# Kernel optimization log

Hardware: AMD Instinct MI355X
Metric: run time of the kernel (lower is better)

Reference implementation:

```python
import jax, jax.numpy as jnp
import numpy as np
from jax import lax

B, L, D, VOCAB = 4, 256, 256, 29


def conv1d(x, w, b, pad, stride=1):
    # x: (B, C, Len), w: (O, I, K)
    y = lax.conv_general_dilated(x, w, (stride,), [pad], dimension_numbers=('NCH', 'OIH', 'NCH'))
    return y + b[None, :, None]


def setup_inputs() -> dict:
    key = jax.random.key(0)
    ks = jax.random.split(key, 14)
    n = lambda k, shape: jax.random.normal(k, shape, jnp.float32) * 0.05
    return {
        'prot_data1': jax.random.randint(ks[0], (B, L), 0, VOCAB),
        'prot_data2': jax.random.randint(ks[1], (B, L), 0, VOCAB),
        'emb': n(ks[2], (VOCAB, D)),
        'w0': n(ks[3], (D, D, 4)), 'b0': jnp.zeros((D,), jnp.float32),
        'w1': n(ks[4], (D, D, 8)), 'b1': jnp.zeros((D,), jnp.float32),
        'w2': n(ks[5], (D, D, 12)), 'b2': jnp.zeros((D,), jnp.float32),
        'ja1_w': n(ks[6], (D, D)), 'ja1_b': jnp.zeros((D,), jnp.float32),
        'ja2_w': n(ks[7], (D, D)), 'ja2_b': jnp.zeros((D,), jnp.float32),
        'rc_w': n(ks[8], (64, 1, 4)), 'rc_b': jnp.zeros((64,), jnp.float32),
        'fc1_w': n(ks[9], (64 * 32, 600)), 'fc1_b': jnp.zeros((600,), jnp.float32),
        'fc2_w': n(ks[10], (600, 300)), 'fc2_b': jnp.zeros((300,), jnp.float32),
        'fc3_w': n(ks[11], (300, 1)), 'fc3_b': jnp.zeros((1,), jnp.float32),
    }


def reference(prot_data1, prot_data2, emb, w0, b0, w1, b1, w2, b2,
              ja1_w, ja1_b, ja2_w, ja2_b, rc_w, rc_b,
              fc1_w, fc1_b, fc2_w, fc2_b, fc3_w, fc3_b):
    lrelu = lambda x: jnp.where(x >= 0, x, 0.1 * x)

    def encode(tok):
        x = emb[tok]  # (B, L, D); dim 1 is treated as conv channels, as in original
        x = jax.nn.relu(conv1d(x, w0, b0, (1, 2)))
        x = jax.nn.relu(conv1d(x, w1, b1, (3, 4)))
        x = jax.nn.relu(conv1d(x, w2, b2, (5, 6)))
        return x  # (B, L, D), length preserved

    e1 = encode(prot_data1)
    e2 = encode(prot_data2)

    q = jax.nn.relu(e1) @ ja1_w + ja1_b  # (B, L, D)
    k = jax.nn.relu(e2) @ ja2_w + ja2_b  # (B, L, D)
    inter = jax.nn.sigmoid(jnp.einsum('bij,bkj->bik', q, k))  # (B, L, L)
    inter = inter / jnp.sum(inter, axis=(1, 2), keepdims=True)

    # bilinear cross-attention pooling: tanh outer product weighted by inter
    pp = jnp.tanh(e1[:, :, None, :] * e2[:, None, :, :])  # (B, L, L, D)
    pooled = jnp.einsum('bikj,bik->bj', pp, inter)  # (B, D)

    h = lrelu(conv1d(pooled[:, None, :], rc_w, rc_b, (1, 1), stride=2))  # (B, 64, 128)
    h = h.reshape(h.shape[0], 64, 32, 4).max(axis=-1)  # MaxPool1d(4,4) -> (B, 64, 32)
    h = h.reshape(h.shape[0], 64 * 32)
    h = lrelu(h @ fc1_w + fc1_b)
    h = lrelu(h @ fc2_w + fc2_b)
    affn = h @ fc3_w + fc3_b  # (B, 1)
    return (inter, affn)
```

## Files before the change

kernel.cpp:

```cpp
#include <hip/hip_runtime.h>
#include <hip/hip_bf16.h>

typedef unsigned short u16;
typedef unsigned int u32;
typedef short s8v __attribute__((ext_vector_type(8)));
typedef float f32x16 __attribute__((ext_vector_type(16)));

constexpr int B = 4, L = 256, D = 256;
constexpr size_t SZ = (size_t)B * L * D;

constexpr int XROWS = 272;
constexpr size_t XT_PLANE = (size_t)8 * XROWS * 256;

constexpr size_t OFF_E    = 0;
constexpr size_t OFF_S    = 2 * SZ;
constexpr size_t OFF_EBF  = 3 * SZ;
constexpr size_t OFF_XA   = 4 * SZ;
constexpr size_t OFF_XB   = OFF_XA + 278528;
constexpr size_t OFF_WB   = OFF_XB + 278528;
constexpr size_t OFF_WJ   = OFF_WB + 1572864;
constexpr size_t OFF_QK   = OFF_WJ + 131072;
constexpr size_t OFF_BS   = OFF_QK + 262144;
constexpr size_t OFF_PP   = OFF_BS + 256;
constexpr size_t OFF_POOL = OFF_PP + 524288;
constexpr size_t OFF_H    = OFF_POOL + 1024;
constexpr size_t OFF_F1P  = OFF_H + 8192;
constexpr size_t OFF_F2P  = OFF_F1P + 76800;

constexpr size_t WB_L1 = 0;
constexpr size_t WB_L2 = (size_t)4 * 2 * 65536;
constexpr size_t WB_L3 = WB_L2 + (size_t)8 * 2 * 65536;

__device__ __forceinline__ float sig_fast(float x) {
  return __fdividef(1.0f, 1.0f + __expf(-x));
}
__device__ __forceinline__ float lrelu(float x) { return x >= 0.0f ? x : 0.1f * x; }

__device__ __forceinline__ void split_bf16(float v, u16& h, u16& l) {
  __bf16 hb = (__bf16)v;
  float hf = (float)hb;
  __bf16 lb = (__bf16)(v - hf);
  h = __builtin_bit_cast(u16, hb);
  l = __builtin_bit_cast(u16, lb);
}
__device__ __forceinline__ u16 to_bf16(float v) {
  return __builtin_bit_cast(u16, (__bf16)v);
}

__device__ __forceinline__ s8v lds16_8al(const u16* p) {
  union { uint2 u[2]; s8v v; } r;
  r.u[0] = *(const uint2*)p;
  r.u[1] = *(const uint2*)(p + 4);
  return r.v;
}

__global__ __launch_bounds__(256) void k_prepall(const int* __restrict__ t1,
                                                 const int* __restrict__ t2,
                                                 const float* __restrict__ emb,
                                                 const float* __restrict__ w0,
                                                 const float* __restrict__ w1,
                                                 const float* __restrict__ w2,
                                                 const float* __restrict__ jw1,
                                                 const float* __restrict__ jw2,
                                                 u16* __restrict__ xa,
                                                 u16* __restrict__ xb,
                                                 u16* __restrict__ wb,
                                                 u16* __restrict__ wj) {
  __shared__ float st[32][129];
  int blk = blockIdx.x;
  int t = threadIdx.x;
  if (blk < 64) {
    int gid = blk * 256 + t;
    int plane = gid >> 13, rem = gid & 8191;
    int pb = rem >> 10, rem2 = rem & 1023;
    int row16 = rem2 >> 6, cc = rem2 & 63;
    int row = row16 < 8 ? row16 : 256 + row16;
    u16* dst = plane ? xb : xa;
    *(ushort4*)(dst + (size_t)pb * (XROWS * 256) + (size_t)row * 256 + cc * 4) =
        make_ushort4(0, 0, 0, 0);
  } else if (blk < 896) {
    int b2 = blk - 64;
    if (b2 < 768) {
      const float* w; u16* dst; int K, lblk;
      if (b2 < 128) { w = w0; dst = wb + WB_L1; K = 4; lblk = b2; }
      else if (b2 < 384) { w = w1; dst = wb + WB_L2; K = 8; lblk = b2 - 128; }
      else { w = w2; dst = wb + WB_L3; K = 12; lblk = b2 - 384; }
      int q = lblk >> 5, ig = lblk & 31, oc = t;
      union { u16 us[8]; uint4 v; } H, Lo;
#pragma unroll
      for (int e = 0; e < 8; ++e) {
        float v = w[((size_t)oc * 256 + ig * 8 + e) * K + q];
        split_bf16(v, H.us[e], Lo.us[e]);
      }
      size_t d = (size_t)(q * 2) * 65536 + (size_t)ig * 2048 + (size_t)oc * 8;
      *(uint4*)(dst + d) = H.v;
      *(uint4*)(dst + d + 65536) = Lo.v;
    } else {
      int lblk = b2 - 768;
      int kg = lblk & 31, p = lblk >> 5;
      const float* W = p ? jw2 : jw1;
      int n = t;
      union { u16 us[8]; uint4 v; } H, Lo;
#pragma unroll
      for (int e = 0; e < 8; ++e) {
        float v = W[(size_t)(kg * 8 + e) * 256 + n];
        split_bf16(v, H.us[e], Lo.us[e]);
      }
      size_t d = (size_t)(p * 2) * 65536 + ((size_t)kg * 256 + n) * 8;
      *(uint4*)(wj + d) = H.v;
      *(uint4*)(wj + d + 65536) = Lo.v;
    }
  } else {
    int lb = blk - 896;
    int dt = lb & 1, lt = (lb >> 1) & 7, pb = lb >> 4;
    int l0 = lt * 32, d0 = dt * 128;
    const int* tok = (pb >> 2) ? t2 : t1;
    int c = t & 127, rq = t >> 7;
#pragma unroll 4
    for (int rr = 0; rr < 16; ++rr) {
      int r = rr * 2 + rq;
      int tv = tok[(pb & 3) * 256 + l0 + r];
      st[r][c] = emb[(size_t)tv * 256 + d0 + c];
    }
    __syncthreads();
    int dloc = t >> 1, lq = t & 1;
    size_t rbase = (size_t)pb * (XROWS * 256) + (size_t)(8 + d0 + dloc) * 256 + l0 + lq * 16;
#pragma unroll
    for (int lh = 0; lh < 4; ++lh) {
      u16 hb[4];
#pragma unroll
      for (int cc = 0; cc < 4; ++cc)
        hb[cc] = to_bf16(st[lq * 16 + lh * 4 + cc][dloc]);
      *(ushort4*)(xa + rbase + lh * 4) = make_ushort4(hb[0], hb[1], hb[2], hb[3]);
    }
  }
}

template <int K, int P, int OUTMODE>
__global__ __launch_bounds__(256, 4) void k_cmf(const u16* __restrict__ xh,
                                                const u16* __restrict__ wb,
                                                const float* __restrict__ bias,
                                                u16* __restrict__ yh,
                                                float* __restrict__ eout,
                                                u16* __restrict__ ebf) {
  __shared__ u16 xs[12480];

  int blk = blockIdx.x;
  int jt = blk & 7, oct = (blk >> 3) & 7, pb = blk >> 6;
  int oc0 = oct * 32, j0 = jt * 32;
  int tid = threadIdx.x;
  int lane = tid & 63, wv = tid >> 6;
  int l31 = lane & 31, lhi = lane >> 5;

  {
    const u32* sh = (const u32*)(xh + (size_t)pb * (XROWS * 256) + (size_t)j0 * 256);
    u32* xd = (u32*)xs;
    for (int idx = tid; idx < 3072; idx += 256) {
      int r = idx >> 6, c2 = (idx & 63) * 2;
      *(uint2*)(xd + r * 130 + c2) = *(const uint2*)(sh + (size_t)r * 128 + c2);
    }
  }
  __syncthreads();

  f32x16 acc = {};
  size_t abase = (size_t)(oc0 + l31) * 8 + (size_t)(wv * 8 + lhi) * 2048;
  int ib0 = wv * 64 + 8 * lhi;

  for (int q = 0; q < K; ++q) {
    int jr = l31 + q + (8 - P);
    const u16* bh0 = xs + jr * 260 + ib0;
    size_t aq = (size_t)q * 131072 + abase;
#pragma unroll
    for (int ic = 0; ic < 4; ++ic) {
      s8v ah = *(const s8v*)(wb + aq + ic * 4096);
      s8v al = *(const s8v*)(wb + aq + 65536 + ic * 4096);
      s8v bh = lds16_8al(bh0 + ic * 16);
      acc = __builtin_amdgcn_mfma_f32_32x32x16_bf16(ah, bh, acc, 0, 0, 0);
      acc = __builtin_amdgcn_mfma_f32_32x32x16_bf16(al, bh, acc, 0, 0, 0);
    }
  }

  __syncthreads();
  float* cd = (float*)xs;
  int j = l31;
  if (wv > 0) {
#pragma unroll
    for (int r = 0; r < 16; ++r) {
      int ocr = (r & 3) + 8 * (r >> 2) + 4 * lhi;
      cd[(wv - 1) * 1024 + ocr * 32 + j] = acc[r];
    }
  }
  __syncthreads();
  if (wv == 0) {
#pragma unroll
    for (int r = 0; r < 16; ++r) {
      int ocr = (r & 3) + 8 * (r >> 2) + 4 * lhi;
      int idx = ocr * 32 + j;
      float s = acc[r] + cd[idx] + cd[1024 + idx] + cd[2048 + idx] + bias[oc0 + ocr];
      cd[3072 + ocr * 33 + j] = fmaxf(s, 0.0f);
    }
  }
  __syncthreads();

  if constexpr (OUTMODE == 0) {
    int jj = tid & 31, oq = tid >> 5;
    u16 hb[4];
#pragma unroll
    for (int c2 = 0; c2 < 4; ++c2)
      hb[c2] = to_bf16(cd[3072 + (oq * 4 + c2) * 33 + jj]);
    size_t ro = (size_t)pb * (XROWS * 256) + (size_t)(8 + j0 + jj) * 256 + oc0 + oq * 4;
    *(ushort4*)(yh + ro) = make_ushort4(hb[0], hb[1], hb[2], hb[3]);
  } else {
    int jj = tid & 31, oq = tid >> 5;
#pragma unroll
    for (int c2 = 0; c2 < 4; ++c2)
      eout[(size_t)pb * 65536 + (size_t)(oc0 + oq * 4 + c2) * 256 + j0 + jj] =
          cd[3072 + (oq * 4 + c2) * 33 + jj];
    int ocl = tid >> 3, dg = tid & 7;
    u16 hb[4];
#pragma unroll
    for (int c2 = 0; c2 < 4; ++c2)
      hb[c2] = to_bf16(cd[3072 + ocl * 33 + dg * 4 + c2]);
    size_t ro2 = ((size_t)pb * 256 + oc0 + ocl) * 256 + j0 + dg * 4;
    *(ushort4*)(ebf + ro2) = make_ushort4(hb[0], hb[1], hb[2], hb[3]);
  }
}

__global__ __launch_bounds__(256) void k_jam(const u16* __restrict__ ebf,
                                             const u16* __restrict__ wj,
                                             const float* __restrict__ b1,
                                             const float* __restrict__ b2,
                                             u16* __restrict__ qk) {
  __shared__ float cd[3072 + 1056];
  int blk = blockIdx.x;
  int nt = blk & 7, it = (blk >> 3) & 7, pb = blk >> 6;
  int p = pb >> 2;
  int i0 = it * 32, n0 = nt * 32;
  int tid = threadIdx.x, wv = tid >> 6, lane = tid & 63;
  int l31 = lane & 31, lhi = lane >> 5;

  const u16* eh = ebf + ((size_t)pb * 256 + i0 + l31) * 256 + lhi * 8;
  const u16* wjh = wj + (size_t)(p * 2) * 65536;

  f32x16 acc = {};
#pragma unroll
  for (int c = 0; c < 4; ++c) {
    int kc = wv * 4 + c;
    int kg = kc * 2 + lhi;
    s8v ah = *(const s8v*)(eh + kc * 16);
    s8v bh = *(const s8v*)(wjh + ((size_t)kg * 256 + n0 + l31) * 8);
    s8v bl = *(const s8v*)(wjh + 65536 + ((size_t)kg * 256 + n0 + l31) * 8);
    acc = __builtin_amdgcn_mfma_f32_32x32x16_bf16(ah, bh, acc, 0, 0, 0);
    acc = __builtin_amdgcn_mfma_f32_32x32x16_bf16(ah, bl, acc, 0, 0, 0);
  }

  if (wv > 0) {
#pragma unroll
    for (int r = 0; r < 16; ++r) {
      int row = (r & 3) + 8 * (r >> 2) + 4 * lhi;
      cd[(wv - 1) * 1024 + row * 32 + l31] = acc[r];
    }
  }
  __syncthreads();
  if (wv == 0) {
    float bv = (p ? b2 : b1)[n0 + l31];
#pragma unroll
    for (int r = 0; r < 16; ++r) {
      int row = (r & 3) + 8 * (r >> 2) + 4 * lhi;
      int idx = row * 32 + l31;
      cd[3072 + row * 33 + l31] = acc[r] + cd[idx] + cd[1024 + idx] + cd[2048 + idx] + bv;
    }
  }
  __syncthreads();

  int row = tid & 31, c8 = tid >> 5;
  u16 hb[4];
#pragma unroll
  for (int cc = 0; cc < 4; ++cc)
    hb[cc] = to_bf16(cd[3072 + row * 33 + c8 * 4 + cc]);
  size_t ro = ((size_t)pb * 256 + i0 + row) * 256 + n0 + c8 * 4;
  *(ushort4*)(qk + ro) = make_ushort4(hb[0], hb[1], hb[2], hb[3]);
}

__global__ __launch_bounds__(256) void k_scoresm(const u16* __restrict__ qk,
                                                 float* __restrict__ S,
                                                 float* __restrict__ bsums) {
  __shared__ float cd[3072 + 1056];
  int blk = blockIdx.x;
  int jt = blk & 7, it = (blk >> 3) & 7, b = blk >> 6;
  int i0 = it * 32, j0 = jt * 32;
  int tid = threadIdx.x, wv = tid >> 6, lane = tid & 63;
  int l31 = lane & 31, lhi = lane >> 5;

  const u16* qh = qk + ((size_t)b * 256 + i0 + l31) * 256 + lhi * 8;
  const u16* kh = qk + ((size_t)(4 + b) * 256 + j0 + l31) * 256 + lhi * 8;

  f32x16 acc = {};
#pragma unroll
  for (int c = 0; c < 4; ++c) {
    int kc = wv * 4 + c;
    s8v a = *(const s8v*)(qh + kc * 16);
    s8v bb = *(const s8v*)(kh + kc * 16);
    acc = __builtin_amdgcn_mfma_f32_32x32x16_bf16(a, bb, acc, 0, 0, 0);
  }

  if (wv > 0) {
#pragma unroll
    for (int r = 0; r < 16; ++r) {
      int row = (r & 3) + 8 * (r >> 2) + 4 * lhi;
      cd[(wv - 1) * 1024 + row * 32 + l31] = acc[r];
    }
  }
  __syncthreads();
  if (wv == 0) {
    float psum = 0.0f;
#pragma unroll
    for (int r = 0; r < 16; ++r) {
      int row = (r & 3) + 8 * (r >> 2) + 4 * lhi;
      int idx = row * 32 + l31;
      float s = sig_fast(acc[r] + cd[idx] + cd[1024 + idx] + cd[2048 + idx]);
      psum += s;
      cd[3072 + row * 33 + l31] = s;
    }
    for (int off = 32; off; off >>= 1) psum += __shfl_down(psum, off, 64);
    if (lane == 0) bsums[blk] = psum;
  }
  __syncthreads();

  int row = tid & 31, c8 = tid >> 5;
  float4 v;
  v.x = cd[3072 + row * 33 + c8 * 4 + 0];
  v.y = cd[3072 + row * 33 + c8 * 4 + 1];
  v.z = cd[3072 + row * 33 + c8 * 4 + 2];
  v.w = cd[3072 + row * 33 + c8 * 4 + 3];
  *(float4*)(S + ((size_t)b * 256 + i0 + row) * 256 + j0 + c8 * 4) = v;
}

__global__ __launch_bounds__(256) void k_norm(const float* __restrict__ S,
                                              const float* __restrict__ bsums,
                                              float* __restrict__ inter_out) {
  int blk = blockIdx.x;
  int b = blk >> 6;
  __shared__ float inv_s;
  int t = threadIdx.x;
  if (t < 64) {
    float v = bsums[b * 64 + t];
    for (int off = 32; off; off >>= 1) v += __shfl_down(v, off, 64);
    if (t == 0) inv_s = 1.0f / v;
  }
  __syncthreads();
  float inv = inv_s;
  size_t base = (size_t)blk * 1024 + (size_t)t * 4;
  float4 v = *(const float4*)(S + base);
  v.x *= inv; v.y *= inv; v.z *= inv; v.w *= inv;
  *(float4*)(inter_out + base) = v;
}

__global__ __launch_bounds__(256) void k_pool(const float* __restrict__ e1,
                                              const float* __restrict__ e2,
                                              const float* __restrict__ S,
                                              const float* __restrict__ bsums,
                                              float* __restrict__ pp) {
  int blk = blockIdx.x;
  int kch = blk & 15, ich = (blk >> 4) & 31, b = blk >> 9;
  int d = threadIdx.x, i0 = ich * 8, k0 = kch * 16;
  __shared__ float s2[16][8];
  __shared__ float red[128];
  __shared__ float ssp_s, tot_s;
  int t = threadIdx.x;
  if (t < 64) {
    float v = bsums[b * 64 + t];
    for (int off = 32; off; off >>= 1) v += __shfl_down(v, off, 64);
    if (t == 0) tot_s = v;
  }
  if (t < 128) {
    int ii = t >> 4, kk = t & 15;
    float v = S[((size_t)(b * 256 + i0 + ii)) * 256 + k0 + kk];
    s2[kk][ii] = 2.0f * v;
    red[t] = v;
  }
  __syncthreads();
  for (int st = 64; st; st >>= 1) {
    if (t < st) red[t] += red[t + st];
    __syncthreads();
  }
  if (t == 0) ssp_s = red[0];
  __syncthreads();

  constexpr float C2L = 2.8853900817779268f;
  float ev2[8];
#pragma unroll
  for (int ii = 0; ii < 8; ++ii)
    ev2[ii] = e1[((size_t)(b * L + i0 + ii)) * D + d] * C2L;

  float a0 = 0.f, a1 = 0.f, a2 = 0.f, a3 = 0.f;
  for (int kk = 0; kk < 16; ++kk) {
    float e2v = e2[((size_t)(b * L + k0 + kk)) * D + d];
    float s2r[8];
    *(float4*)&s2r[0] = *(const float4*)&s2[kk][0];
    *(float4*)&s2r[4] = *(const float4*)&s2[kk][4];
#pragma unroll
    for (int ii = 0; ii < 8; ++ii) {
      float r = __builtin_amdgcn_rcpf(__builtin_exp2f(ev2[ii] * e2v) + 1.0f);
      if ((ii & 3) == 0) a0 = fmaf(r, s2r[ii], a0);
      else if ((ii & 3) == 1) a1 = fmaf(r, s2r[ii], a1);
      else if ((ii & 3) == 2) a2 = fmaf(r, s2r[ii], a2);
      else a3 = fmaf(r, s2r[ii], a3);
    }
  }
  float res = (ssp_s - (a0 + a1 + a2 + a3)) * (1.0f / tot_s);
  pp[(((size_t)b * 32 + ich) * 16 + kch) * 256 + d] = res;
}

__global__ __launch_bounds__(256) void k_poolcomb(const float* __restrict__ pp,
                                                  float* __restrict__ pooled) {
  int blk = blockIdx.x;
  int dt = blk & 7, b = blk >> 3;
  int t = threadIdx.x, dl = t & 31, mg = t >> 5;
  int d = dt * 32 + dl;
  float s = 0.f;
#pragma unroll
  for (int m = 0; m < 64; ++m)
    s += pp[((size_t)b * 512 + mg * 64 + m) * 256 + d];
  __shared__ float red[8][32];
  red[mg][dl] = s;
  __syncthreads();
  if (mg == 0) {
    float tot = red[0][dl] + red[1][dl] + red[2][dl] + red[3][dl] +
                red[4][dl] + red[5][dl] + red[6][dl] + red[7][dl];
    pooled[b * 256 + d] = tot;
  }
}

__global__ __launch_bounds__(256) void k_head1(const float* __restrict__ pooled,
                                               const float* __restrict__ rcw,
                                               const float* __restrict__ rcb,
                                               float* __restrict__ h) {
  int ms = blockIdx.x;
  __shared__ float spb[4][258];
  int t = threadIdx.x;
#pragma unroll
  for (int s = 0; s < 4; ++s) {
    int idx = s * 256 + t;
    spb[idx >> 8][(idx & 255) + 1] = pooled[idx];
  }
  if (t < 4) { spb[t][0] = 0.0f; spb[t][257] = 0.0f; }
  __syncthreads();
  int b = t >> 6, c = t & 63;
  float w0 = rcw[c * 4 + 0], w1 = rcw[c * 4 + 1], w2 = rcw[c * 4 + 2], w3 = rcw[c * 4 + 3];
  float bias = rcb[c];
#pragma unroll
  for (int mm = 0; mm < 4; ++mm) {
    int m = ms * 4 + mm;
    float mx = -1e30f;
#pragma unroll
    for (int r = 0; r < 4; ++r) {
      int p2 = 2 * (4 * m + r);
      float y = bias;
      y = fmaf(w0, spb[b][p2], y);
      y = fmaf(w1, spb[b][p2 + 1], y);
      y = fmaf(w2, spb[b][p2 + 2], y);
      y = fmaf(w3, spb[b][p2 + 3], y);
      mx = fmaxf(mx, lrelu(y));
    }
    h[(size_t)(b * 64 + c) * 32 + m] = mx;
  }
}

__global__ __launch_bounds__(256) void k_fc1(const float* __restrict__ h,
                                             const float* __restrict__ w,
                                             float* __restrict__ f1p) {
  int blk = blockIdx.x;
  int ich = blk & 31, ot = blk >> 5;
  int t = threadIdx.x, ol = t & 63, b = t >> 6;
  int o = ot * 64 + ol;
  int oc_ = o < 600 ? o : 599;
  const float* hb = h + (size_t)b * 2048 + ich * 64;
  const float* wb = w + (size_t)(ich * 64) * 600 + oc_;
  float a0 = 0.f, a1 = 0.f, a2 = 0.f, a3 = 0.f;
#pragma unroll 4
  for (int i = 0; i < 64; i += 4) {
    a0 = fmaf(hb[i], wb[(size_t)i * 600], a0);
    a1 = fmaf(hb[i + 1], wb[(size_t)(i + 1) * 600], a1);
    a2 = fmaf(hb[i + 2], wb[(size_t)(i + 2) * 600], a2);
    a3 = fmaf(hb[i + 3], wb[(size_t)(i + 3) * 600], a3);
  }
  if (o < 600) f1p[((size_t)ich * 4 + b) * 600 + o] = a0 + a1 + a2 + a3;
}

__global__ __launch_bounds__(256) void k_fc2(const float* __restrict__ f1p,
                                             const float* __restrict__ fc1b,
                                             const float* __restrict__ w,
                                             float* __restrict__ f2p) {
  int blk = blockIdx.x;
  int is = blk & 7, ot = blk >> 3;
  __shared__ float h1s[4][76];
  int t = threadIdx.x;
  for (int e = t; e < 300; e += 256) {
    int bb = e / 75, ii = e % 75;
    int i = is * 75 + ii;
    float s = fc1b[i];
#pragma unroll
    for (int ich = 0; ich < 32; ++ich) s += f1p[((size_t)ich * 4 + bb) * 600 + i];
    h1s[bb][ii] = lrelu(s);
  }
  __syncthreads();
  int ol = t & 63, b = t >> 6;
  int o = ot * 64 + ol, oc_ = o < 300 ? o : 299;
  const float* wb = w + (size_t)(is * 75) * 300 + oc_;
  float a0 = 0.f, a1 = 0.f, a2 = 0.f;
#pragma unroll 5
  for (int ii = 0; ii < 75; ii += 3) {
    a0 = fmaf(h1s[b][ii], wb[(size_t)ii * 300], a0);
    a1 = fmaf(h1s[b][ii + 1], wb[(size_t)(ii + 1) * 300], a1);
    a2 = fmaf(h1s[b][ii + 2], wb[(size_t)(ii + 2) * 300], a2);
  }
  if (o < 300) f2p[((size_t)is * 4 + b) * 300 + o] = a0 + a1 + a2;
}

__global__ __launch_bounds__(1024) void k_fc3f(const float* __restrict__ f2p,
                                               const float* __restrict__ fc2b,
                                               const float* __restrict__ w3,
                                               const float* __restrict__ fc3b,
                                               float* __restrict__ out) {
  __shared__ float h2s[4][304];
  int t = threadIdx.x;
  for (int e = t; e < 1200; e += 1024) {
    int o = e % 300, b = e / 300;
    float s = fc2b[o];
#pragma unroll
    for (int is = 0; is < 8; ++is) s += f2p[((size_t)is * 4 + b) * 300 + o];
    h2s[b][o] = lrelu(s);
  }
  __syncthreads();
  int wv = t >> 6, l = t & 63;
  if (wv < 4) {
    float s = 0.f;
#pragma unroll
    for (int m = 0; m < 5; ++m) {
      int i = m * 64 + l;
      if (i < 300) s = fmaf(h2s[wv][i], w3[i], s);
    }
    for (int off = 32; off; off >>= 1) s += __shfl_down(s, off, 64);
    if (l == 0) out[262144 + wv] = s + fc3b[0];
  }
}

extern "C" void kernel_launch(void* const* d_in, const int* in_sizes, int n_in,
                              void* d_out, int out_size, void* d_ws, size_t ws_size,
                              hipStream_t stream) {
  float* ws = (float*)d_ws;
  const int* p1 = (const int*)d_in[0];
  const int* p2 = (const int*)d_in[1];
  const float* emb  = (const float*)d_in[2];
  const float* w0   = (const float*)d_in[3];
  const float* b0   = (const float*)d_in[4];
  const float* w1   = (const float*)d_in[5];
  const float* b1   = (const float*)d_in[6];
  const float* w2   = (const float*)d_in[7];
  const float* b2   = (const float*)d_in[8];
  const float* ja1w = (const float*)d_in[9];
  const float* ja1b = (const float*)d_in[10];
  const float* ja2w = (const float*)d_in[11];
  const float* ja2b = (const float*)d_in[12];
  const float* rcw  = (const float*)d_in[13];
  const float* rcb  = (const float*)d_in[14];
  const float* fc1w = (const float*)d_in[15];
  const float* fc1b = (const float*)d_in[16];
  const float* fc2w = (const float*)d_in[17];
  const float* fc2b = (const float*)d_in[18];
  const float* fc3w = (const float*)d_in[19];
  const float* fc3b = (const float*)d_in[20];
  float* out = (float*)d_out;

  u16* xa  = (u16*)(ws + OFF_XA);
  u16* xb  = (u16*)(ws + OFF_XB);
  u16* wbu = (u16*)(ws + OFF_WB);
  u16* wju = (u16*)(ws + OFF_WJ);
  u16* ebf = (u16*)(ws + OFF_EBF);
  u16* qk  = (u16*)(ws + OFF_QK);

  k_prepall<<<1024, 256, 0, stream>>>(p1, p2, emb, w0, w1, w2, ja1w, ja2w, xa, xb, wbu, wju);

  k_cmf<4, 1, 0><<<512, 256, 0, stream>>>(xa, wbu + WB_L1, b0, xb, nullptr, nullptr);
  k_cmf<8, 3, 0><<<512, 256, 0, stream>>>(xb, wbu + WB_L2, b1, xa, nullptr, nullptr);
  k_cmf<12, 5, 1><<<512, 256, 0, stream>>>(xa, wbu + WB_L3, b2, nullptr, ws + OFF_E, ebf);

  k_jam<<<512, 256, 0, stream>>>(ebf, wju, ja1b, ja2b, qk);
  k_scoresm<<<256, 256, 0, stream>>>(qk, ws + OFF_S, ws + OFF_BS);
  k_norm<<<256, 256, 0, stream>>>(ws + OFF_S, ws + OFF_BS, out);

  k_pool<<<2048, 256, 0, stream>>>(ws + OFF_E, ws + OFF_E + SZ, ws + OFF_S, ws + OFF_BS,
                                   ws + OFF_PP);
  k_poolcomb<<<32, 256, 0, stream>>>(ws + OFF_PP, ws + OFF_POOL);

  k_head1<<<8, 256, 0, stream>>>(ws + OFF_POOL, rcw, rcb, ws + OFF_H);
  k_fc1<<<320, 256, 0, stream>>>(ws + OFF_H, fc1w, ws + OFF_F1P);
  k_fc2<<<40, 256, 0, stream>>>(ws + OFF_F1P, fc1b, fc2w, ws + OFF_F2P);
  k_fc3f<<<1, 1024, 0, stream>>>(ws + OFF_F2P, fc2b, fc3w, fc3b, out);
}
```

Before: 101.1 us.

## Fuse normalization into pooling kernel and restructure conv LDS staging per wave

Removes the separate k_norm launch by having k_pool write the normalized interaction matrix for the tile it already reads. In k_cmf, each wave now loads only its own input-channel slice into a private LDS region, so the post-load block barrier is replaced by a local waitcnt. The epilogue writes results straight from registers instead of bouncing them through a second LDS transpose. Launch bounds drop from 4 to 2 blocks per CU, which gives more registers but may reduce occupancy, and the direct per-element ebf/eout stores are less coalesced.

```diff
diff --git a/kernel.cpp b/kernel.cpp
--- a/kernel.cpp
+++ b/kernel.cpp
@@ -137,13 +137,14 @@
 }
 
 template <int K, int P, int OUTMODE>
-__global__ __launch_bounds__(256, 4) void k_cmf(const u16* __restrict__ xh,
+__global__ __launch_bounds__(256, 2) void k_cmf(const u16* __restrict__ xh,
                                                 const u16* __restrict__ wb,
                                                 const float* __restrict__ bias,
                                                 u16* __restrict__ yh,
                                                 float* __restrict__ eout,
                                                 u16* __restrict__ ebf) {
-  __shared__ u16 xs[12480];
+  __shared__ u16 xsl[4 * 3264];
+  __shared__ float cd[3072];
 
   int blk = blockIdx.x;
   int jt = blk & 7, oct = (blk >> 3) & 7, pb = blk >> 6;
@@ -153,22 +154,25 @@
   int l31 = lane & 31, lhi = lane >> 5;
 
   {
-    const u32* sh = (const u32*)(xh + (size_t)pb * (XROWS * 256) + (size_t)j0 * 256);
-    u32* xd = (u32*)xs;
-    for (int idx = tid; idx < 3072; idx += 256) {
-      int r = idx >> 6, c2 = (idx & 63) * 2;
-      *(uint2*)(xd + r * 130 + c2) = *(const uint2*)(sh + (size_t)r * 128 + c2);
-    }
-  }
-  __syncthreads();
+    const u16* src = xh + (size_t)pb * (XROWS * 256) + (size_t)j0 * 256 + wv * 64;
+    u16* dst = xsl + wv * 3264;
+#pragma unroll
+    for (int it2 = 0; it2 < 12; ++it2) {
+      int e = it2 * 64 + lane;
+      int r = e >> 4, c4 = (e & 15) * 4;
+      *(uint2*)(dst + r * 68 + c4) = *(const uint2*)(src + (size_t)r * 256 + c4);
+    }
+  }
+  asm volatile("s_waitcnt lgkmcnt(0)" ::: "memory");
+  __builtin_amdgcn_sched_barrier(0);
 
   f32x16 acc = {};
   size_t abase = (size_t)(oc0 + l31) * 8 + (size_t)(wv * 8 + lhi) * 2048;
-  int ib0 = wv * 64 + 8 * lhi;
+  const u16* wslice = xsl + wv * 3264 + 8 * lhi;
 
   for (int q = 0; q < K; ++q) {
     int jr = l31 + q + (8 - P);
-    const u16* bh0 = xs + jr * 260 + ib0;
+    const u16* bh0 = wslice + jr * 68;
     size_t aq = (size_t)q * 131072 + abase;
 #pragma unroll
     for (int ic = 0; ic < 4; ++ic) {
@@ -180,49 +184,39 @@
     }
   }
 
-  __syncthreads();
-  float* cd = (float*)xs;
-  int j = l31;
   if (wv > 0) {
 #pragma unroll
     for (int r = 0; r < 16; ++r) {
       int ocr = (r & 3) + 8 * (r >> 2) + 4 * lhi;
-      cd[(wv - 1) * 1024 + ocr * 32 + j] = acc[r];
+      cd[(wv - 1) * 1024 + ocr * 32 + l31] = acc[r];
     }
   }
   __syncthreads();
   if (wv == 0) {
+    float v[16];
 #pragma unroll
     for (int r = 0; r < 16; ++r) {
       int ocr = (r & 3) + 8 * (r >> 2) + 4 * lhi;
-      int idx = ocr * 32 + j;
-      float s = acc[r] + cd[idx] + cd[1024 + idx] + cd[2048 + idx] + bias[oc0 + ocr];
-      cd[3072 + ocr * 33 + j] = fmaxf(s, 0.0f);
-    }
-  }
-  __syncthreads();
-
-  if constexpr (OUTMODE == 0) {
-    int jj = tid & 31, oq = tid >> 5;
-    u16 hb[4];
-#pragma unroll
-    for (int c2 = 0; c2 < 4; ++c2)
-      hb[c2] = to_bf16(cd[3072 + (oq * 4 + c2) * 33 + jj]);
-    size_t ro = (size_t)pb * (XROWS * 256) + (size_t)(8 + j0 + jj) * 256 + oc0 + oq * 4;
-    *(ushort4*)(yh + ro) = make_ushort4(hb[0], hb[1], hb[2], hb[3]);
-  } else {
-    int jj = tid & 31, oq = tid >> 5;
-#pragma unroll
-    for (int c2 = 0; c2 < 4; ++c2)
-      eout[(size_t)pb * 65536 + (size_t)(oc0 + oq * 4 + c2) * 256 + j0 + jj] =
-          cd[3072 + (oq * 4 + c2) * 33 + jj];
-    int ocl = tid >> 3, dg = tid & 7;
-    u16 hb[4];
-#pragma unroll
-    for (int c2 = 0; c2 < 4; ++c2)
-      hb[c2] = to_bf16(cd[3072 + ocl * 33 + dg * 4 + c2]);
-    size_t ro2 = ((size_t)pb * 256 + oc0 + ocl) * 256 + j0 + dg * 4;
-    *(ushort4*)(ebf + ro2) = make_ushort4(hb[0], hb[1], hb[2], hb[3]);
+      int idx = ocr * 32 + l31;
+      v[r] = fmaxf(acc[r] + cd[idx] + cd[1024 + idx] + cd[2048 + idx] + bias[oc0 + ocr], 0.0f);
+    }
+    if constexpr (OUTMODE == 0) {
+      size_t ro = (size_t)pb * (XROWS * 256) + (size_t)(8 + j0 + l31) * 256 + oc0 + 4 * lhi;
+#pragma unroll
+      for (int rq = 0; rq < 4; ++rq) {
+        *(ushort4*)(yh + ro + 8 * rq) =
+            make_ushort4(to_bf16(v[rq * 4 + 0]), to_bf16(v[rq * 4 + 1]),
+                         to_bf16(v[rq * 4 + 2]), to_bf16(v[rq * 4 + 3]));
+      }
+    } else {
+#pragma unroll
+      for (int r = 0; r < 16; ++r) {
+        int ocr = (r & 3) + 8 * (r >> 2) + 4 * lhi;
+        size_t eo = (size_t)pb * 65536 + (size_t)(oc0 + ocr) * 256 + j0 + l31;
+        eout[eo] = v[r];
+        ebf[((size_t)pb * 256 + oc0 + ocr) * 256 + j0 + l31] = to_bf16(v[r]);
+      }
+    }
   }
 }
 
@@ -336,30 +330,11 @@
   *(float4*)(S + ((size_t)b * 256 + i0 + row) * 256 + j0 + c8 * 4) = v;
 }
 
-__global__ __launch_bounds__(256) void k_norm(const float* __restrict__ S,
-                                              const float* __restrict__ bsums,
-                                              float* __restrict__ inter_out) {
-  int blk = blockIdx.x;
-  int b = blk >> 6;
-  __shared__ float inv_s;
-  int t = threadIdx.x;
-  if (t < 64) {
-    float v = bsums[b * 64 + t];
-    for (int off = 32; off; off >>= 1) v += __shfl_down(v, off, 64);
-    if (t == 0) inv_s = 1.0f / v;
-  }
-  __syncthreads();
-  float inv = inv_s;
-  size_t base = (size_t)blk * 1024 + (size_t)t * 4;
-  float4 v = *(const float4*)(S + base);
-  v.x *= inv; v.y *= inv; v.z *= inv; v.w *= inv;
-  *(float4*)(inter_out + base) = v;
-}
-
 __global__ __launch_bounds__(256) void k_pool(const float* __restrict__ e1,
                                               const float* __restrict__ e2,
                                               const float* __restrict__ S,
                                               const float* __restrict__ bsums,
+                                              float* __restrict__ inter_out,
                                               float* __restrict__ pp) {
   int blk = blockIdx.x;
   int kch = blk & 15, ich = (blk >> 4) & 31, b = blk >> 9;
@@ -368,16 +343,17 @@
   __shared__ float red[128];
   __shared__ float ssp_s, tot_s;
   int t = threadIdx.x;
+  int ii = t >> 4, kk = t & 15;
+  float sv = 0.0f;
   if (t < 64) {
     float v = bsums[b * 64 + t];
     for (int off = 32; off; off >>= 1) v += __shfl_down(v, off, 64);
     if (t == 0) tot_s = v;
   }
   if (t < 128) {
-    int ii = t >> 4, kk = t & 15;
-    float v = S[((size_t)(b * 256 + i0 + ii)) * 256 + k0 + kk];
-    s2[kk][ii] = 2.0f * v;
-    red[t] = v;
+    sv = S[((size_t)(b * 256 + i0 + ii)) * 256 + k0 + kk];
+    s2[kk][ii] = 2.0f * sv;
+    red[t] = sv;
   }
   __syncthreads();
   for (int st = 64; st; st >>= 1) {
@@ -387,28 +363,32 @@
   if (t == 0) ssp_s = red[0];
   __syncthreads();
 
+  float invt = 1.0f / tot_s;
+  if (t < 128)
+    inter_out[((size_t)(b * 256 + i0 + ii)) * 256 + k0 + kk] = sv * invt;
+
   constexpr float C2L = 2.8853900817779268f;
   float ev2[8];
 #pragma unroll
-  for (int ii = 0; ii < 8; ++ii)
-    ev2[ii] = e1[((size_t)(b * L + i0 + ii)) * D + d] * C2L;
+  for (int i2 = 0; i2 < 8; ++i2)
+    ev2[i2] = e1[((size_t)(b * L + i0 + i2)) * D + d] * C2L;
 
   float a0 = 0.f, a1 = 0.f, a2 = 0.f, a3 = 0.f;
-  for (int kk = 0; kk < 16; ++kk) {
-    float e2v = e2[((size_t)(b * L + k0 + kk)) * D + d];
+  for (int k2 = 0; k2 < 16; ++k2) {
+    float e2v = e2[((size_t)(b * L + k0 + k2)) * D + d];
     float s2r[8];
-    *(float4*)&s2r[0] = *(const float4*)&s2[kk][0];
-    *(float4*)&s2r[4] = *(const float4*)&s2[kk][4];
-#pragma unroll
-    for (int ii = 0; ii < 8; ++ii) {
-      float r = __builtin_amdgcn_rcpf(__builtin_exp2f(ev2[ii] * e2v) + 1.0f);
-      if ((ii & 3) == 0) a0 = fmaf(r, s2r[ii], a0);
-      else if ((ii & 3) == 1) a1 = fmaf(r, s2r[ii], a1);
-      else if ((ii & 3) == 2) a2 = fmaf(r, s2r[ii], a2);
-      else a3 = fmaf(r, s2r[ii], a3);
-    }
-  }
-  float res = (ssp_s - (a0 + a1 + a2 + a3)) * (1.0f / tot_s);
+    *(float4*)&s2r[0] = *(const float4*)&s2[k2][0];
+    *(float4*)&s2r[4] = *(const float4*)&s2[k2][4];
+#pragma unroll
+    for (int i2 = 0; i2 < 8; ++i2) {
+      float r = __builtin_amdgcn_rcpf(__builtin_exp2f(ev2[i2] * e2v) + 1.0f);
+      if ((i2 & 3) == 0) a0 = fmaf(r, s2r[i2], a0);
+      else if ((i2 & 3) == 1) a1 = fmaf(r, s2r[i2], a1);
+      else if ((i2 & 3) == 2) a2 = fmaf(r, s2r[i2], a2);
+      else a3 = fmaf(r, s2r[i2], a3);
+    }
+  }
+  float res = (ssp_s - (a0 + a1 + a2 + a3)) * invt;
   pp[(((size_t)b * 32 + ich) * 16 + kch) * 256 + d] = res;
 }
 
@@ -588,10 +568,9 @@
 
   k_jam<<<512, 256, 0, stream>>>(ebf, wju, ja1b, ja2b, qk);
   k_scoresm<<<256, 256, 0, stream>>>(qk, ws + OFF_S, ws + OFF_BS);
-  k_norm<<<256, 256, 0, stream>>>(ws + OFF_S, ws + OFF_BS, out);
 
   k_pool<<<2048, 256, 0, stream>>>(ws + OFF_E, ws + OFF_E + SZ, ws + OFF_S, ws + OFF_BS,
-                                   ws + OFF_PP);
+                                   out, ws + OFF_PP);
   k_poolcomb<<<32, 256, 0, stream>>>(ws + OFF_PP, ws + OFF_POOL);
 
   k_head1<<<8, 256, 0, stream>>>(ws + OFF_POOL, rcw, rcb, ws + OFF_H);
```

Result: faster. 98.14 us (-3.0%).
